# Kernel tuning notes

Measured on AMD Instinct MI355X. Metric: run time of the kernel, lower is better.

The kernel has to match this reference:

```python
import jax, jax.numpy as jnp
import numpy as np

R, B, F, H, C = 32, 2048, 512, 1024, 100  # n_rules, batch, n_fea, 2*n_fea, n_cls


def setup_inputs() -> dict:
    key = jax.random.key(0)
    ks = jax.random.split(key, 10)
    sc = lambda k, shape, fan: (jax.random.normal(k, shape, jnp.float32) / np.float32(np.sqrt(fan)))
    return {
        "data": jax.random.normal(ks[0], (B, F), jnp.float32),
        "proto": jax.random.normal(ks[1], (R, F), jnp.float32),
        "var": jax.random.uniform(ks[2], (R, F), jnp.float32, 0.5, 1.5),
        "fs_w1": sc(ks[3], (F, H), F), "fs_b1": jnp.zeros((H,), jnp.float32),
        "fs_w2": sc(ks[4], (H, F), H), "fs_b2": jnp.zeros((F,), jnp.float32),
        "fs_w3": sc(ks[5], (F, 1), F), "fs_b3": jnp.zeros((1,), jnp.float32),
        "cq_w1": sc(ks[6], (R, F, H), F), "cq_b1": jnp.zeros((R, H), jnp.float32),
        "cq_w2": sc(ks[7], (R, H, F), H), "cq_b2": jnp.zeros((R, F), jnp.float32),
        "cq_w3": sc(ks[8], (R, F, C), F), "cq_b3": jnp.zeros((R, C), jnp.float32),
        "is_train": 1,
    }


def reference(data, proto, var, fs_w1, fs_b1, fs_w2, fs_b2, fs_w3, fs_b3,
              cq_w1, cq_b1, cq_w2, cq_b2, cq_w3, cq_b3, is_train):
    # Gaussian fuzzy membership per rule: [R, B, F]
    fuzzy = jnp.exp(-(data[None, :, :] - proto[:, None, :]) ** 2
                    / (2.0 * var[:, None, :] ** 2))
    # shared fire-strength MLP applied per rule
    h = jax.nn.relu(jnp.einsum('rbf,fh->rbh', fuzzy, fs_w1) + fs_b1)
    h = jax.nn.relu(jnp.einsum('rbh,hf->rbf', h, fs_w2) + fs_b2)
    fs_logits = (jnp.einsum('rbf,fo->rbo', h, fs_w3) + fs_b3)[..., 0]  # [R, B]
    fire = jax.nn.softmax(fs_logits.T, axis=1)  # [B, R], softmax over rules
    # per-rule consequent MLPs on raw data (grouped GEMMs)
    g = jax.nn.relu(jnp.einsum('bf,rfh->rbh', data, cq_w1) + cq_b1[:, None, :])
    g = jax.nn.relu(jnp.einsum('rbh,rhf->rbf', g, cq_w2) + cq_b2[:, None, :])
    logits = jnp.einsum('rbf,rfc->rbc', g, cq_w3) + cq_b3[:, None, :]  # [R, B, C]
    # softmax-weighted expert sum, then class softmax
    out = jnp.einsum('br,rbc->bc', fire, logits)  # [B, C]
    return jax.nn.softmax(out, axis=1)
```

## Files before the change

kernel.cpp:

```cpp
#include <hip/hip_runtime.h>

typedef __attribute__((ext_vector_type(8))) short short8;
typedef __attribute__((ext_vector_type(4))) float f32x4;

__device__ __forceinline__ unsigned short f2bf(float f) {
    union { float f; unsigned u; } v; v.f = f;
    unsigned r = v.u + 0x7FFFu + ((v.u >> 16) & 1u);
    return (unsigned short)(r >> 16);
}
__device__ __forceinline__ float bf2f(unsigned short u) {
    union { unsigned u; float f; } v; v.u = ((unsigned)u) << 16;
    return v.f;
}

__global__ __launch_bounds__(256)
void cvt_bf16_kernel(const float* __restrict__ X, unsigned short* __restrict__ Y, int n4) {
    int i = blockIdx.x * 256 + threadIdx.x;
    if (i >= n4) return;
    float4 v = ((const float4*)X)[i];
    ushort4 o; o.x = f2bf(v.x); o.y = f2bf(v.y); o.z = f2bf(v.z); o.w = f2bf(v.w);
    ((ushort4*)Y)[i] = o;
}

__global__ __launch_bounds__(256)
void transpose_kernel(const float* __restrict__ X, unsigned short* __restrict__ Y,
                      int K, int N, int Np) {
    __shared__ float tile[32][33];
    int g = blockIdx.z;
    const float* Xg = X + (long)g * K * N;
    unsigned short* Yg = Y + (long)g * Np * K;
    int k0 = blockIdx.x * 32, n0 = blockIdx.y * 32;
    int tx = threadIdx.x & 31, ty = threadIdx.x >> 5;
#pragma unroll
    for (int i = 0; i < 4; ++i) {
        int kk = ty + i * 8;
        int n = n0 + tx;
        tile[kk][tx] = (n < N) ? Xg[(long)(k0 + kk) * N + n] : 0.0f;
    }
    __syncthreads();
#pragma unroll
    for (int i = 0; i < 4; ++i) {
        int nn = ty + i * 8;
        Yg[(long)(n0 + nn) * K + k0 + tx] = f2bf(tile[tx][nn]);
    }
}

__global__ __launch_bounds__(128)
void fuzzy_kernel(const float* __restrict__ data, const float* __restrict__ proto,
                  const float* __restrict__ var, unsigned short* __restrict__ fuzzy,
                  int r0) {
    int rb = blockIdx.x;
    int r = r0 + (rb >> 11), b = rb & 2047;
    int f = threadIdx.x * 4;
    float4 d = *(const float4*)(data + (long)b * 512 + f);
    float4 p = *(const float4*)(proto + (long)r * 512 + f);
    float4 w = *(const float4*)(var + (long)r * 512 + f);
    ushort4 o;
    float x;
    x = d.x - p.x; o.x = f2bf(__expf(-(x * x) / (2.f * w.x * w.x)));
    x = d.y - p.y; o.y = f2bf(__expf(-(x * x) / (2.f * w.y * w.y)));
    x = d.z - p.z; o.z = f2bf(__expf(-(x * x) / (2.f * w.z * w.z)));
    x = d.w - p.w; o.w = f2bf(__expf(-(x * x) / (2.f * w.w * w.w)));
    *(ushort4*)(fuzzy + (long)rb * 512 + f) = o;
}

template<int EPI, bool RELU>
__global__ __launch_bounds__(256, 2)
void gemm_kernel(const unsigned short* __restrict__ A,
                 const unsigned short* __restrict__ Bt,
                 const float* __restrict__ bias,
                 void* __restrict__ Cptr,
                 const float* __restrict__ w3,
                 float* __restrict__ fslog,
                 int nM, int nN, int K,
                 long sAg, long sBg, long sCg, int sBiasG, int biasN) {
    unsigned tot = gridDim.x;
    unsigned bid = blockIdx.x;
    unsigned sw = (tot & 7u) == 0 ? (bid & 7u) * (tot >> 3) + (bid >> 3) : bid;
    unsigned pg = (unsigned)nM * (unsigned)nN;
    unsigned g = sw / pg;
    unsigned rem = sw - g * pg;
    unsigned mt_ = rem / (unsigned)nN;
    unsigned nt_ = rem - mt_ * (unsigned)nN;
    const int N = nN * 128;
    A += (long)g * sAg;
    Bt += (long)g * sBg;
    bias += (long)g * sBiasG;
    const int m0 = (int)mt_ * 128;
    const int n0 = (int)nt_ * 128;

    __shared__ __align__(16) unsigned short ldsA[128 * 32];
    __shared__ __align__(16) unsigned short ldsB[128 * 32];

    const int tid = threadIdx.x;
    const int lane = tid & 63;
    const int w = tid >> 6;
    const int wm = w >> 1, wn = w & 1;
    const int r16 = lane & 15, kg = lane >> 4;

    f32x4 acc[4][4];
#pragma unroll
    for (int i = 0; i < 4; ++i)
#pragma unroll
        for (int j = 0; j < 4; ++j) {
            f32x4 z = {0.f, 0.f, 0.f, 0.f};
            acc[i][j] = z;
        }

    for (int k0 = 0; k0 < K; k0 += 32) {
#pragma unroll
        for (int j = 0; j < 2; ++j) {
            int t = j * 256 + tid;
            int row = t >> 2, kc = (t & 3) * 8;
            const unsigned short* ga = A + (long)(m0 + row) * K + k0 + kc;
            __builtin_amdgcn_global_load_lds(
                (const __attribute__((address_space(1))) void*)ga,
                (__attribute__((address_space(3))) void*)(ldsA + (j * 256 + w * 64) * 8),
                16, 0, 0);
            const unsigned short* gb = Bt + (long)(n0 + row) * K + k0 + kc;
            __builtin_amdgcn_global_load_lds(
                (const __attribute__((address_space(1))) void*)gb,
                (__attribute__((address_space(3))) void*)(ldsB + (j * 256 + w * 64) * 8),
                16, 0, 0);
        }
        __syncthreads();
        short8 aF[4], bF[4];
#pragma unroll
        for (int mt = 0; mt < 4; ++mt)
            aF[mt] = *(const short8*)(ldsA + (wm * 64 + mt * 16 + r16) * 32 + kg * 8);
#pragma unroll
        for (int nt = 0; nt < 4; ++nt)
            bF[nt] = *(const short8*)(ldsB + (wn * 64 + nt * 16 + r16) * 32 + kg * 8);
#pragma unroll
        for (int mt = 0; mt < 4; ++mt)
#pragma unroll
            for (int nt = 0; nt < 4; ++nt)
                acc[mt][nt] = __builtin_amdgcn_mfma_f32_16x16x32_bf16(
                    aF[mt], bF[nt], acc[mt][nt], 0, 0, 0);
        __syncthreads();
    }

    if constexpr (EPI == 1) {
        float w3v[4], bv[4];
#pragma unroll
        for (int nt = 0; nt < 4; ++nt) {
            int col = n0 + wn * 64 + nt * 16 + r16;
            w3v[nt] = w3[col];
            bv[nt] = bias[col];
        }
#pragma unroll
        for (int mt = 0; mt < 4; ++mt) {
#pragma unroll
            for (int j = 0; j < 4; ++j) {
                float p = 0.f;
#pragma unroll
                for (int nt = 0; nt < 4; ++nt) {
                    float v = acc[mt][nt][j] + bv[nt];
                    if (RELU) v = fmaxf(v, 0.f);
                    p += v * w3v[nt];
                }
                p += __shfl_xor(p, 1, 64);
                p += __shfl_xor(p, 2, 64);
                p += __shfl_xor(p, 4, 64);
                p += __shfl_xor(p, 8, 64);
                if (r16 == 0) {
                    int row = m0 + wm * 64 + mt * 16 + kg * 4 + j;
                    atomicAdd(&fslog[row], p);
                }
            }
        }
    } else {
#pragma unroll
        for (int nt = 0; nt < 4; ++nt) {
            int col = n0 + wn * 64 + nt * 16 + r16;
            float bv = (col < biasN) ? bias[col] : 0.f;
#pragma unroll
            for (int mt = 0; mt < 4; ++mt) {
#pragma unroll
                for (int j = 0; j < 4; ++j) {
                    int row = m0 + wm * 64 + mt * 16 + kg * 4 + j;
                    float v = acc[mt][nt][j] + bv;
                    if (RELU) v = fmaxf(v, 0.f);
                    if constexpr (EPI == 0)
                        ((unsigned short*)Cptr)[(long)g * sCg + (long)row * N + col] = f2bf(v);
                    else
                        ((float*)Cptr)[(long)g * sCg + (long)row * N + col] = v;
                }
            }
        }
    }
}

__global__ __launch_bounds__(256)
void fire_kernel(const float* __restrict__ fslog, float* __restrict__ fire) {
    int b = blockIdx.x * 256 + threadIdx.x;
    float v[32];
    float mx = -1e30f;
#pragma unroll
    for (int r = 0; r < 32; ++r) { v[r] = fslog[r * 2048 + b]; mx = fmaxf(mx, v[r]); }
    float s = 0.f;
#pragma unroll
    for (int r = 0; r < 32; ++r) { v[r] = __expf(v[r] - mx); s += v[r]; }
    float inv = 1.f / s;
#pragma unroll
    for (int r = 0; r < 32; ++r) fire[b * 32 + r] = v[r] * inv;
}

__global__ __launch_bounds__(128)
void accum_kernel(const float* __restrict__ logits, const float* __restrict__ fire,
                  float* __restrict__ mix, int r0, int NR, int first) {
    int b = blockIdx.x, c = threadIdx.x;
    float acc = first ? 0.f : mix[b * 128 + c];
    for (int r = 0; r < NR; ++r)
        acc += fire[b * 32 + r0 + r] * logits[((long)r * 2048 + b) * 128 + c];
    mix[b * 128 + c] = acc;
}

__global__ __launch_bounds__(128)
void softmax_out_kernel(const float* __restrict__ mix, float* __restrict__ out) {
    int b = blockIdx.x, c = threadIdx.x;
    __shared__ float redm[2], reds[2];
    float val = (c < 100) ? mix[b * 128 + c] : -1e30f;
    float m = val;
#pragma unroll
    for (int off = 32; off; off >>= 1) m = fmaxf(m, __shfl_xor(m, off, 64));
    int lane = c & 63, wv = c >> 6;
    if (lane == 0) redm[wv] = m;
    __syncthreads();
    m = fmaxf(redm[0], redm[1]);
    float e = (c < 100) ? __expf(val - m) : 0.f;
    float s = e;
#pragma unroll
    for (int off = 32; off; off >>= 1) s += __shfl_xor(s, off, 64);
    if (lane == 0) reds[wv] = s;
    __syncthreads();
    s = reds[0] + reds[1];
    if (c < 100) out[b * 100 + c] = e / s;
}

extern "C" void kernel_launch(void* const* d_in, const int* in_sizes, int n_in,
                              void* d_out, int out_size, void* d_ws, size_t ws_size,
                              hipStream_t stream) {
    const float* data  = (const float*)d_in[0];
    const float* proto = (const float*)d_in[1];
    const float* var   = (const float*)d_in[2];
    const float* fs_w1 = (const float*)d_in[3];
    const float* fs_b1 = (const float*)d_in[4];
    const float* fs_w2 = (const float*)d_in[5];
    const float* fs_b2 = (const float*)d_in[6];
    const float* fs_w3 = (const float*)d_in[7];
    const float* cq_w1 = (const float*)d_in[9];
    const float* cq_b1 = (const float*)d_in[10];
    const float* cq_w2 = (const float*)d_in[11];
    const float* cq_b2 = (const float*)d_in[12];
    const float* cq_w3 = (const float*)d_in[13];
    const float* cq_b3 = (const float*)d_in[14];
    float* out = (float*)d_out;

    const size_t PERSIST = 2097152 + 1048576 + 1048576 + 262144 + 262144 + 1048576;
    const size_t PER_RULE_P2 = 1048576 + 1048576 + 131072 + 2097152;
    auto need = [&](int p1r, int p2r) -> size_t {
        size_t logitsC = (size_t)p2r * 2048 * 128 * 4;
        size_t R0 = (size_t)p1r * 2048 * 512 * 2;
        size_t r0p2 = (size_t)p2r * PER_RULE_P2;
        if (r0p2 > R0) R0 = r0p2;
        size_t R1 = (size_t)p1r * 2048 * 1024 * 2;
        size_t g1b = (size_t)p2r * 2048 * 1024 * 2;
        if (g1b > R1) R1 = g1b;
        return PERSIST + logitsC + R0 + R1;
    };
    int p1r = 32, p2r = 16;
    while (need(p1r, p2r) > ws_size && p1r > 2) { p1r >>= 1; p2r >>= 1; }

    char* ws = (char*)d_ws;
    size_t off = 0;
    auto take = [&](size_t bytes) { char* p = ws + off; off += bytes; return p; };
    unsigned short* data_bf = (unsigned short*)take(2097152);
    unsigned short* w1t     = (unsigned short*)take(1048576);
    unsigned short* w2t     = (unsigned short*)take(1048576);
    float*          fslog   = (float*)take(262144);
    float*          fire    = (float*)take(262144);
    float*          mix     = (float*)take(1048576);
    float*          logitsC = (float*)take((size_t)p2r * 2048 * 128 * 4);
    size_t R0sz = (size_t)p1r * 2048 * 512 * 2;
    { size_t t = (size_t)p2r * PER_RULE_P2; if (t > R0sz) R0sz = t; }
    char* R0 = take(R0sz);
    size_t R1sz = (size_t)p1r * 2048 * 1024 * 2;
    char* R1 = take(R1sz);

    unsigned short* cF   = (unsigned short*)R0;
    unsigned short* cW1t = (unsigned short*)R0;
    unsigned short* cW2t = (unsigned short*)(R0 + (size_t)p2r * 1048576);
    unsigned short* cW3t = (unsigned short*)(R0 + (size_t)p2r * 2097152);
    unsigned short* g2   = (unsigned short*)(R0 + (size_t)p2r * 2097152 + (size_t)p2r * 131072);
    unsigned short* h1   = (unsigned short*)R1;
    unsigned short* g1   = (unsigned short*)R1;

    cvt_bf16_kernel<<<1024, 256, 0, stream>>>(data, data_bf, 262144);
    transpose_kernel<<<dim3(16, 32, 1), 256, 0, stream>>>(fs_w1, w1t, 512, 1024, 1024);
    transpose_kernel<<<dim3(32, 16, 1), 256, 0, stream>>>(fs_w2, w2t, 1024, 512, 512);
    hipMemsetAsync(fslog, 0, 262144, stream);

    for (int ch = 0; ch < 32 / p1r; ++ch) {
        const int r0 = ch * p1r;
        fuzzy_kernel<<<p1r * 2048, 128, 0, stream>>>(data, proto, var, cF, r0);
        gemm_kernel<0, true><<<p1r * 16 * 8, 256, 0, stream>>>(
            cF, w1t, fs_b1, h1, nullptr, nullptr,
            p1r * 16, 8, 512, 0, 0, 0, 0, 1024);
        gemm_kernel<1, true><<<p1r * 16 * 4, 256, 0, stream>>>(
            h1, w2t, fs_b2, nullptr, fs_w3, fslog + (long)r0 * 2048,
            p1r * 16, 4, 1024, 0, 0, 0, 0, 512);
    }
    fire_kernel<<<8, 256, 0, stream>>>(fslog, fire);

    for (int ch = 0; ch < 32 / p2r; ++ch) {
        const int r0 = ch * p2r;
        transpose_kernel<<<dim3(16, 32, p2r), 256, 0, stream>>>(
            cq_w1 + (long)r0 * 512 * 1024, cW1t, 512, 1024, 1024);
        transpose_kernel<<<dim3(32, 16, p2r), 256, 0, stream>>>(
            cq_w2 + (long)r0 * 1024 * 512, cW2t, 1024, 512, 512);
        transpose_kernel<<<dim3(16, 4, p2r), 256, 0, stream>>>(
            cq_w3 + (long)r0 * 512 * 100, cW3t, 512, 100, 128);
        gemm_kernel<0, true><<<16 * 8 * p2r, 256, 0, stream>>>(
            data_bf, cW1t, cq_b1 + (long)r0 * 1024, g1, nullptr, nullptr,
            16, 8, 512, 0, (long)1024 * 512, (long)2048 * 1024, 1024, 1024);
        gemm_kernel<0, true><<<16 * 4 * p2r, 256, 0, stream>>>(
            g1, cW2t, cq_b2 + (long)r0 * 512, g2, nullptr, nullptr,
            16, 4, 1024, (long)2048 * 1024, (long)512 * 1024, (long)2048 * 512, 512, 512);
        gemm_kernel<2, false><<<16 * 1 * p2r, 256, 0, stream>>>(
            g2, cW3t, cq_b3 + (long)r0 * 100, logitsC, nullptr, nullptr,
            16, 1, 512, (long)2048 * 512, (long)128 * 512, (long)2048 * 128, 100, 100);
        accum_kernel<<<2048, 128, 0, stream>>>(logitsC, fire, mix, r0, p2r, ch == 0);
    }
    softmax_out_kernel<<<2048, 128, 0, stream>>>(mix, out);
}
```

Before: 549.8 us.

## Add 256x256-tile GEMM with async global-to-LDS four-stage ring pipeline

Adds a new 512-thread GEMM kernel that computes 256x256 output tiles. It stages K-slices straight into LDS through global_load_lds into a four-slot ring with XOR-swizzled layout, and waits on vmcnt before each barrier so loads overlap MFMA work. The fire-strength MLP GEMMs and the first two consequent GEMMs now use it, while the narrow final GEMM stays on the old 128-tile kernel, which loses its unused fused epilogue. Larger tiles raise data reuse and cut grid size, at the cost of 128 KB of LDS and heavy register use per block, which may limit occupancy.

```diff
diff --git a/kernel.cpp b/kernel.cpp
--- a/kernel.cpp
+++ b/kernel.cpp
@@ -64,14 +64,159 @@
     *(ushort4*)(fuzzy + (long)rb * 512 + f) = o;
 }
 
+#define RING_WAIT_BARRIER(n)                                        \
+    asm volatile("s_waitcnt vmcnt(" #n ")" ::: "memory");           \
+    __builtin_amdgcn_sched_barrier(0);                              \
+    __builtin_amdgcn_s_barrier();                                   \
+    __builtin_amdgcn_sched_barrier(0);
+
+template<int EPI, bool RELU>
+__global__ __launch_bounds__(512, 2)
+void gemm256_kernel(const unsigned short* __restrict__ A,
+                    const unsigned short* __restrict__ Bt,
+                    const float* __restrict__ bias,
+                    void* __restrict__ Cptr,
+                    const float* __restrict__ w3,
+                    float* __restrict__ fslog,
+                    int nM, int nN, int K,
+                    long sAg, long sBg, long sCg, int sBiasG) {
+    unsigned tot = gridDim.x, bid = blockIdx.x;
+    unsigned sw = (bid & 7u) * (tot >> 3) + (bid >> 3);
+    unsigned pg = (unsigned)(nM * nN);
+    unsigned g = sw / pg;
+    unsigned rem = sw - g * pg;
+    const int m0 = (int)(rem / (unsigned)nN) * 256;
+    const int n0 = (int)(rem % (unsigned)nN) * 256;
+    const int N = nN * 256;
+    A += (long)g * sAg; Bt += (long)g * sBg; bias += (long)g * sBiasG;
+
+    __shared__ __align__(16) unsigned short lds[8][8192];
+
+    const int tid = threadIdx.x;
+    const int lane = tid & 63;
+    const int w = tid >> 6;
+    const int wm = w >> 2, wn = w & 3;
+    const int r16 = lane & 15, kg = lane >> 4;
+
+    f32x4 acc[8][4];
+#pragma unroll
+    for (int i = 0; i < 8; ++i)
+#pragma unroll
+        for (int j = 0; j < 4; ++j) {
+            f32x4 z = {0.f, 0.f, 0.f, 0.f};
+            acc[i][j] = z;
+        }
+
+    const int nsteps = K >> 5;
+
+    auto STAGE = [&](int slot, int kt) {
+        const int k0 = kt << 5;
+#pragma unroll
+        for (int j = 0; j < 2; ++j) {
+            int f = j * 512 + tid;
+            int row = f >> 2, sl = f & 3;
+            int kk = (sl ^ ((row >> 1) & 3)) << 3;
+            const unsigned short* ga = A + (long)(m0 + row) * K + k0 + kk;
+            __builtin_amdgcn_global_load_lds(
+                (const __attribute__((address_space(1))) void*)ga,
+                (__attribute__((address_space(3))) void*)(&lds[slot][0] + (j * 512 + w * 64) * 8),
+                16, 0, 0);
+            const unsigned short* gb = Bt + (long)(n0 + row) * K + k0 + kk;
+            __builtin_amdgcn_global_load_lds(
+                (const __attribute__((address_space(1))) void*)gb,
+                (__attribute__((address_space(3))) void*)(&lds[4 + slot][0] + (j * 512 + w * 64) * 8),
+                16, 0, 0);
+        }
+    };
+
+    auto COMPUTE = [&](int slot) {
+        short8 aF[8], bF[4];
+#pragma unroll
+        for (int mt = 0; mt < 8; ++mt) {
+            int R = wm * 128 + mt * 16 + r16;
+            aF[mt] = *(const short8*)(&lds[slot][0] + R * 32 + ((kg ^ ((R >> 1) & 3)) << 3));
+        }
+#pragma unroll
+        for (int nt = 0; nt < 4; ++nt) {
+            int R = wn * 64 + nt * 16 + r16;
+            bF[nt] = *(const short8*)(&lds[4 + slot][0] + R * 32 + ((kg ^ ((R >> 1) & 3)) << 3));
+        }
+        __builtin_amdgcn_s_setprio(1);
+#pragma unroll
+        for (int mt = 0; mt < 8; ++mt)
+#pragma unroll
+            for (int nt = 0; nt < 4; ++nt)
+                acc[mt][nt] = __builtin_amdgcn_mfma_f32_16x16x32_bf16(
+                    aF[mt], bF[nt], acc[mt][nt], 0, 0, 0);
+        __builtin_amdgcn_s_setprio(0);
+        asm volatile("" ::: "memory");
+        __builtin_amdgcn_s_barrier();
+        __builtin_amdgcn_sched_barrier(0);
+    };
+
+    STAGE(0, 0); STAGE(1, 1); STAGE(2, 2);
+    for (int t = 0; t <= nsteps - 3; ++t) {
+        if (t + 3 < nsteps) STAGE((t + 3) & 3, t + 3);
+        RING_WAIT_BARRIER(8);
+        COMPUTE(t & 3);
+    }
+    { RING_WAIT_BARRIER(4); COMPUTE((nsteps - 2) & 3); }
+    { RING_WAIT_BARRIER(0); COMPUTE((nsteps - 1) & 3); }
+
+    if constexpr (EPI == 1) {
+        float w3v[4], bv[4];
+#pragma unroll
+        for (int nt = 0; nt < 4; ++nt) {
+            int col = n0 + wn * 64 + nt * 16 + r16;
+            w3v[nt] = w3[col];
+            bv[nt] = bias[col];
+        }
+#pragma unroll
+        for (int mt = 0; mt < 8; ++mt) {
+#pragma unroll
+            for (int j = 0; j < 4; ++j) {
+                float p = 0.f;
+#pragma unroll
+                for (int nt = 0; nt < 4; ++nt) {
+                    float v = acc[mt][nt][j] + bv[nt];
+                    if (RELU) v = fmaxf(v, 0.f);
+                    p += v * w3v[nt];
+                }
+                p += __shfl_xor(p, 1, 64);
+                p += __shfl_xor(p, 2, 64);
+                p += __shfl_xor(p, 4, 64);
+                p += __shfl_xor(p, 8, 64);
+                if (r16 == 0) {
+                    int row = m0 + wm * 128 + mt * 16 + kg * 4 + j;
+                    atomicAdd(&fslog[row], p);
+                }
+            }
+        }
+    } else {
+#pragma unroll
+        for (int nt = 0; nt < 4; ++nt) {
+            int col = n0 + wn * 64 + nt * 16 + r16;
+            float bv = bias[col];
+#pragma unroll
+            for (int mt = 0; mt < 8; ++mt) {
+#pragma unroll
+                for (int j = 0; j < 4; ++j) {
+                    int row = m0 + wm * 128 + mt * 16 + kg * 4 + j;
+                    float v = acc[mt][nt][j] + bv;
+                    if (RELU) v = fmaxf(v, 0.f);
+                    ((unsigned short*)Cptr)[(long)g * sCg + (long)row * N + col] = f2bf(v);
+                }
+            }
+        }
+    }
+}
+
 template<int EPI, bool RELU>
 __global__ __launch_bounds__(256, 2)
 void gemm_kernel(const unsigned short* __restrict__ A,
                  const unsigned short* __restrict__ Bt,
                  const float* __restrict__ bias,
                  void* __restrict__ Cptr,
-                 const float* __restrict__ w3,
-                 float* __restrict__ fslog,
                  int nM, int nN, int K,
                  long sAg, long sBg, long sCg, int sBiasG, int biasN) {
     unsigned tot = gridDim.x;
@@ -140,52 +285,21 @@
         __syncthreads();
     }
 
-    if constexpr (EPI == 1) {
-        float w3v[4], bv[4];
-#pragma unroll
-        for (int nt = 0; nt < 4; ++nt) {
-            int col = n0 + wn * 64 + nt * 16 + r16;
-            w3v[nt] = w3[col];
-            bv[nt] = bias[col];
-        }
+#pragma unroll
+    for (int nt = 0; nt < 4; ++nt) {
+        int col = n0 + wn * 64 + nt * 16 + r16;
+        float bv = (col < biasN) ? bias[col] : 0.f;
 #pragma unroll
         for (int mt = 0; mt < 4; ++mt) {
 #pragma unroll
             for (int j = 0; j < 4; ++j) {
-                float p = 0.f;
-#pragma unroll
-                for (int nt = 0; nt < 4; ++nt) {
-                    float v = acc[mt][nt][j] + bv[nt];
-                    if (RELU) v = fmaxf(v, 0.f);
-                    p += v * w3v[nt];
-                }
-                p += __shfl_xor(p, 1, 64);
-                p += __shfl_xor(p, 2, 64);
-                p += __shfl_xor(p, 4, 64);
-                p += __shfl_xor(p, 8, 64);
-                if (r16 == 0) {
-                    int row = m0 + wm * 64 + mt * 16 + kg * 4 + j;
-                    atomicAdd(&fslog[row], p);
-                }
-            }
-        }
-    } else {
-#pragma unroll
-        for (int nt = 0; nt < 4; ++nt) {
-            int col = n0 + wn * 64 + nt * 16 + r16;
-            float bv = (col < biasN) ? bias[col] : 0.f;
-#pragma unroll
-            for (int mt = 0; mt < 4; ++mt) {
-#pragma unroll
-                for (int j = 0; j < 4; ++j) {
-                    int row = m0 + wm * 64 + mt * 16 + kg * 4 + j;
-                    float v = acc[mt][nt][j] + bv;
-                    if (RELU) v = fmaxf(v, 0.f);
-                    if constexpr (EPI == 0)
-                        ((unsigned short*)Cptr)[(long)g * sCg + (long)row * N + col] = f2bf(v);
-                    else
-                        ((float*)Cptr)[(long)g * sCg + (long)row * N + col] = v;
-                }
+                int row = m0 + wm * 64 + mt * 16 + kg * 4 + j;
+                float v = acc[mt][nt][j] + bv;
+                if (RELU) v = fmaxf(v, 0.f);
+                if constexpr (EPI == 0)
+                    ((unsigned short*)Cptr)[(long)g * sCg + (long)row * N + col] = f2bf(v);
+                else
+                    ((float*)Cptr)[(long)g * sCg + (long)row * N + col] = v;
             }
         }
     }
@@ -286,6 +400,7 @@
     { size_t t = (size_t)p2r * PER_RULE_P2; if (t > R0sz) R0sz = t; }
     char* R0 = take(R0sz);
     size_t R1sz = (size_t)p1r * 2048 * 1024 * 2;
+    { size_t t = (size_t)p2r * 2048 * 1024 * 2; if (t > R1sz) R1sz = t; }
     char* R1 = take(R1sz);
 
     unsigned short* cF   = (unsigned short*)R0;
@@ -304,12 +419,12 @@
     for (int ch = 0; ch < 32 / p1r; ++ch) {
         const int r0 = ch * p1r;
         fuzzy_kernel<<<p1r * 2048, 128, 0, stream>>>(data, proto, var, cF, r0);
-        gemm_kernel<0, true><<<p1r * 16 * 8, 256, 0, stream>>>(
+        gemm256_kernel<0, true><<<p1r * 8 * 4, 512, 0, stream>>>(
             cF, w1t, fs_b1, h1, nullptr, nullptr,
-            p1r * 16, 8, 512, 0, 0, 0, 0, 1024);
-        gemm_kernel<1, true><<<p1r * 16 * 4, 256, 0, stream>>>(
+            p1r * 8, 4, 512, 0, 0, 0, 0);
+        gemm256_kernel<1, true><<<p1r * 8 * 2, 512, 0, stream>>>(
             h1, w2t, fs_b2, nullptr, fs_w3, fslog + (long)r0 * 2048,
-            p1r * 16, 4, 1024, 0, 0, 0, 0, 512);
+            p1r * 8, 2, 1024, 0, 0, 0, 0);
     }
     fire_kernel<<<8, 256, 0, stream>>>(fslog, fire);
 
@@ -321,14 +436,14 @@
             cq_w2 + (long)r0 * 1024 * 512, cW2t, 1024, 512, 512);
         transpose_kernel<<<dim3(16, 4, p2r), 256, 0, stream>>>(
             cq_w3 + (long)r0 * 512 * 100, cW3t, 512, 100, 128);
-        gemm_kernel<0, true><<<16 * 8 * p2r, 256, 0, stream>>>(
+        gemm256_kernel<0, true><<<8 * 4 * p2r, 512, 0, stream>>>(
             data_bf, cW1t, cq_b1 + (long)r0 * 1024, g1, nullptr, nullptr,
-            16, 8, 512, 0, (long)1024 * 512, (long)2048 * 1024, 1024, 1024);
-        gemm_kernel<0, true><<<16 * 4 * p2r, 256, 0, stream>>>(
+            8, 4, 512, 0, (long)1024 * 512, (long)2048 * 1024, 1024);
+        gemm256_kernel<0, true><<<8 * 2 * p2r, 512, 0, stream>>>(
             g1, cW2t, cq_b2 + (long)r0 * 512, g2, nullptr, nullptr,
-            16, 4, 1024, (long)2048 * 1024, (long)512 * 1024, (long)2048 * 512, 512, 512);
+            8, 2, 1024, (long)2048 * 1024, (long)512 * 1024, (long)2048 * 512, 512);
         gemm_kernel<2, false><<<16 * 1 * p2r, 256, 0, stream>>>(
-            g2, cW3t, cq_b3 + (long)r0 * 100, logitsC, nullptr, nullptr,
+            g2, cW3t, cq_b3 + (long)r0 * 100, logitsC,
             16, 1, 512, (long)2048 * 512, (long)128 * 512, (long)2048 * 128, 100, 100);
         accum_kernel<<<2048, 128, 0, stream>>>(logitsC, fire, mix, r0, p2r, ch == 0);
     }
```

Result: faster. 536.7 us (-2.4%).
